# Optimization experiments

Measured on AMD Instinct MI355X. Metric: run time of the kernel, lower is better.

## Reference

```python
import jax, jax.numpy as jnp
import numpy as np
from jax import lax

B, T, D = 64, 2048, 80
H = 128          # hidden_dim
H2 = 2 * H       # conv out channels / GRU input / bi-GRU output
L = 2            # gru layers
O = 4            # output_dim


def setup_inputs() -> dict:
    key = jax.random.key(0)
    ks = jax.random.split(key, 16)
    f = lambda k, shape, scale: (jax.random.normal(k, shape) * scale).astype(jnp.float32)
    return {
        "x": f(ks[0], (B, T, D), 1.0),
        # conv branches: PyTorch Conv1d weight layout [out, in, k]
        "conv1_w": f(ks[1], (H2, D, 1), 0.1), "conv1_b": f(ks[2], (H2,), 0.1),
        "conv3_w": f(ks[3], (H2, D, 3), 0.06), "conv3_b": f(ks[4], (H2,), 0.1),
        "conv5_w": f(ks[5], (H2, D, 5), 0.05), "conv5_b": f(ks[6], (H2,), 0.1),
        # skip / head linears: PyTorch Linear weight layout [out, in]
        "fc1_w": f(ks[7], (H2, D), 0.1), "fc1_b": f(ks[8], (H2,), 0.1),
        "fc_w": f(ks[9], (O, H2), 0.06), "fc_b": f(ks[10], (O,), 0.1),
        # stacked bidirectional GRU weights: [layer, dir(0=fwd,1=bwd), 3H, ...]
        # gate order along 3H axis follows PyTorch: reset, update, new
        "gru_wih": f(ks[11], (L, 2, 3 * H, H2), 0.06),
        "gru_whh": f(ks[12], (L, 2, 3 * H, H), 0.08),
        "gru_bih": f(ks[13], (L, 2, 3 * H), 0.05),
        "gru_bhh": f(ks[14], (L, 2, 3 * H), 0.05),
    }


def _conv_relu(xc, w, b, pad):
    # xc: [B, C, T], w: [out, in, k]
    y = lax.conv_general_dilated(xc, w, window_strides=(1,), padding=[(pad, pad)],
                                 dimension_numbers=("NCH", "OIH", "NCH"))
    return jax.nn.relu(y + b[None, :, None])


def _gru_dir(xin, wih, whh, bih, bhh, reverse):
    # xin: [B, T, Din]; PyTorch GRU cell: r,z,n gate order
    Hd = whh.shape[1]
    xg = jnp.einsum("btd,gd->btg", xin, wih) + bih  # [B, T, 3H]
    if reverse:
        xg = xg[:, ::-1]

    def step(h, xt):
        hg = h @ whh.T + bhh                                   # [B, 3H]
        r = jax.nn.sigmoid(xt[:, :Hd] + hg[:, :Hd])
        z = jax.nn.sigmoid(xt[:, Hd:2 * Hd] + hg[:, Hd:2 * Hd])
        n = jnp.tanh(xt[:, 2 * Hd:] + r * hg[:, 2 * Hd:])
        hn = (1.0 - z) * n + z * h
        return hn, hn

    h0 = jnp.zeros((xin.shape[0], Hd), xin.dtype)
    _, hs = lax.scan(step, h0, xg.transpose(1, 0, 2))          # [T, B, H]
    hs = hs.transpose(1, 0, 2)
    return hs[:, ::-1] if reverse else hs


def reference(x, conv1_w, conv1_b, conv3_w, conv3_b, conv5_w, conv5_b,
              fc1_w, fc1_b, fc_w, fc_b, gru_wih, gru_whh, gru_bih, gru_bhh):
    xc = x.transpose(0, 2, 1)                                   # [B, D, T]
    oc = (_conv_relu(xc, conv1_w, conv1_b, 0)
          + _conv_relu(xc, conv3_w, conv3_b, 1)
          + _conv_relu(xc, conv5_w, conv5_b, 2))                # [B, 2H, T]
    h = oc.transpose(0, 2, 1)                                   # [B, T, 2H]

    for l in range(gru_wih.shape[0]):
        fwd = _gru_dir(h, gru_wih[l, 0], gru_whh[l, 0], gru_bih[l, 0], gru_bhh[l, 0], False)
        bwd = _gru_dir(h, gru_wih[l, 1], gru_whh[l, 1], gru_bih[l, 1], gru_bhh[l, 1], True)
        h = jnp.concatenate([fwd, bwd], axis=-1)                # [B, T, 2H]

    output_gru = h + x @ fc1_w.T + fc1_b                        # skip connection
    out = output_gru @ fc_w.T + fc_b                            # [B, T, O]
    return output_gru, out
```

## Files before the change

### kernel.cpp

```cpp
#include <hip/hip_runtime.h>
#include <hip/hip_bf16.h>
#include <hip/hip_fp16.h>

typedef _Float16 f16;
typedef _Float16 h2_t __attribute__((ext_vector_type(2)));
typedef _Float16 h4_t __attribute__((ext_vector_type(4)));
typedef _Float16 h8_t __attribute__((ext_vector_type(8)));
typedef float    f4_t __attribute__((ext_vector_type(4)));

#define B_  64
#define T_  2048
#define BT_ 131072
#define OG_ELEMS 33554432ull

__device__ __forceinline__ void gl_lds16(const void* g, void* lds) {
  __builtin_amdgcn_global_load_lds(
      (const __attribute__((address_space(1))) void*)g,
      (__attribute__((address_space(3))) void*)lds, 16, 0, 0);
}

__device__ __forceinline__ h8_t pack8(const float* p) {
  f4_t a = *(const f4_t*)p;
  f4_t b = *(const f4_t*)(p + 4);
  return h8_t{(f16)a[0], (f16)a[1], (f16)a[2], (f16)a[3],
              (f16)b[0], (f16)b[1], (f16)b[2], (f16)b[3]};
}

__device__ __forceinline__ void kloop128(
    const f16* __restrict__ Ab, int lda,
    const f16* __restrict__ Bb, int ldb,
    int ksteps, f16* As, f16* Bs, f4_t (&acc)[4][4])
{
  const int tid  = threadIdx.x;
  const int wave = tid >> 6, lane = tid & 63;
  const int srow = tid >> 2;
  const int scol = (tid & 3) * 8;
  const int fr   = lane & 15;
  const int kb   = (lane >> 4) * 8;
  const int rA   = (wave >> 1) * 64 + fr;
  const int rB   = (wave & 1) * 64 + fr;

  f16* dA0 = As + wave * 512;
  f16* dA1 = As + 2048 + wave * 512;
  f16* dB0 = Bs + wave * 512;
  f16* dB1 = Bs + 2048 + wave * 512;
  const f16* gA0 = Ab + (size_t)srow * lda + scol;
  const f16* gA1 = Ab + (size_t)(srow + 64) * lda + scol;
  const f16* gB0 = Bb + (size_t)srow * ldb + scol;
  const f16* gB1 = Bb + (size_t)(srow + 64) * ldb + scol;

  for (int kt = 0; kt < ksteps; ++kt) {
    const int ko = kt * 32;
    gl_lds16(gA0 + ko, dA0);
    gl_lds16(gA1 + ko, dA1);
    gl_lds16(gB0 + ko, dB0);
    gl_lds16(gB1 + ko, dB1);
    __syncthreads();
    h8_t af[4], bf[4];
#pragma unroll
    for (int m = 0; m < 4; m++) af[m] = *(const h8_t*)(As + (rA + m * 16) * 32 + kb);
#pragma unroll
    for (int n = 0; n < 4; n++) bf[n] = *(const h8_t*)(Bs + (rB + n * 16) * 32 + kb);
#pragma unroll
    for (int m = 0; m < 4; m++)
#pragma unroll
      for (int n = 0; n < 4; n++)
        acc[m][n] = __builtin_amdgcn_mfma_f32_16x16x32_f16(af[m], bf[n], acc[m][n], 0, 0, 0);
    __syncthreads();
  }
}

__global__ __launch_bounds__(256) void gemm_xT_kernel(
    const f16* __restrict__ A, int lda,
    const f16* __restrict__ Bw, int ldb,
    const float* __restrict__ bias,
    f16* __restrict__ out, int ksteps, int mode)
{
  __shared__ f16 As[4096];
  __shared__ f16 Bs[4096];
  f4_t acc[4][4];
#pragma unroll
  for (int m = 0; m < 4; m++)
#pragma unroll
    for (int n = 0; n < 4; n++) acc[m][n] = f4_t{0.f, 0.f, 0.f, 0.f};

  const f16* Ab = A + (size_t)blockIdx.x * 128 * lda;
  const f16* Bb = Bw + (size_t)blockIdx.y * 128 * ldb;
  kloop128(Ab, lda, Bb, ldb, ksteps, As, Bs, acc);

  const int tid = threadIdx.x, wave = tid >> 6, lane = tid & 63;
  const int col0 = blockIdx.y * 128 + (wave & 1) * 64 + (lane & 15);
  const int row0 = blockIdx.x * 128 + (wave >> 1) * 64 + (lane >> 4) * 4;
  const int b = blockIdx.x >> 4;
#pragma unroll
  for (int n = 0; n < 4; n++) {
    const int col = col0 + n * 16;
    const float bv = bias[col];
    const int g = col >> 7, jj = col & 127;
    const size_t base = (mode == 0)
        ? ((size_t)((b * 3 + g) * 128 + jj)) * 2048
        : ((size_t)((g * 64 + b) * 128 + jj)) * 2048;
#pragma unroll
    for (int m = 0; m < 4; m++) {
      const int row = row0 + m * 16;
      const int t = row & 2047;
      h4_t v = h4_t{(f16)(acc[m][n][0] + bv), (f16)(acc[m][n][1] + bv),
                    (f16)(acc[m][n][2] + bv), (f16)(acc[m][n][3] + bv)};
      *(h4_t*)(out + base + t) = v;
    }
  }
}

__global__ __launch_bounds__(256) void conv3sum_kernel(
    const f16* __restrict__ A5,
    const f16* __restrict__ W5p, const f16* __restrict__ W3p, const f16* __restrict__ W1p,
    const float* __restrict__ b5, const float* __restrict__ b3, const float* __restrict__ b1,
    f16* __restrict__ oc)
{
  __shared__ f16 As[4096];
  __shared__ f16 Bs[4096];
  const int tid = threadIdx.x, wave = tid >> 6, lane = tid & 63;
  const int col0 = blockIdx.y * 128 + (wave & 1) * 64 + (lane & 15);
  const int row0 = blockIdx.x * 128 + (wave >> 1) * 64 + (lane >> 4) * 4;
  const f16* Ab = A5 + (size_t)blockIdx.x * 128 * 480;

  f4_t tot[4][4];
#pragma unroll
  for (int m = 0; m < 4; m++)
#pragma unroll
    for (int n = 0; n < 4; n++) tot[m][n] = f4_t{0.f, 0.f, 0.f, 0.f};

  auto seg = [&](const f16* Wp, int ldb, int ks, int aoff, const float* bias) {
    f4_t acc[4][4];
#pragma unroll
    for (int m = 0; m < 4; m++)
#pragma unroll
      for (int n = 0; n < 4; n++) acc[m][n] = f4_t{0.f, 0.f, 0.f, 0.f};
    kloop128(Ab + aoff, 480, Wp + (size_t)blockIdx.y * 128 * ldb, ldb, ks, As, Bs, acc);
#pragma unroll
    for (int n = 0; n < 4; n++) {
      const float bv = bias[col0 + n * 16];
#pragma unroll
      for (int m = 0; m < 4; m++)
#pragma unroll
        for (int q = 0; q < 4; q++)
          tot[m][n][q] += fmaxf(acc[m][n][q] + bv, 0.f);
    }
  };
  seg(W5p, 480, 15, 0,   b5);
  seg(W3p, 288, 9,  96,  b3);
  seg(W1p, 96,  3,  192, b1);

#pragma unroll
  for (int n = 0; n < 4; n++) {
    const int col = col0 + n * 16;
#pragma unroll
    for (int m = 0; m < 4; m++) {
      const int row = row0 + m * 16;
#pragma unroll
      for (int q = 0; q < 4; q++)
        oc[(size_t)(row + q) * 256 + col] = (f16)tot[m][n][q];
    }
  }
}

__global__ __launch_bounds__(384) void im2col_kernel(
    const float* __restrict__ x, f16* __restrict__ A5)
{
  const int tid = threadIdx.x;
  const int r = tid / 12, c8 = tid % 12;
  const int bt = blockIdx.x * 32 + r;
  const int kg = blockIdx.y;
  const int b = bt >> 11, t = bt & 2047;
  const int ts = t + kg - 2;
  h8_t v = {0, 0, 0, 0, 0, 0, 0, 0};
  if (c8 < 10 && (unsigned)ts < 2048u) {
    const float* src = x + ((size_t)(b << 11) + ts) * 80 + c8 * 8;
    f4_t a = *(const f4_t*)src;
    f4_t bvec = *(const f4_t*)(src + 4);
    v = h8_t{(f16)a[0], (f16)a[1], (f16)a[2], (f16)a[3],
             (f16)bvec[0], (f16)bvec[1], (f16)bvec[2], (f16)bvec[3]};
  }
  *(h8_t*)(A5 + (size_t)bt * 480 + kg * 96 + c8 * 8) = v;
}

__global__ void pack_convw_kernel(
    const float* __restrict__ w1, const float* __restrict__ w3,
    const float* __restrict__ w5, const float* __restrict__ fc1w,
    f16* __restrict__ W5p, f16* __restrict__ W3p, f16* __restrict__ W1p,
    f16* __restrict__ FC1p)
{
  const int col = blockIdx.x;
  const int c = threadIdx.x;
  if (col < 480) {
    const int kg = col / 96, d = col % 96;
    W5p[c * 480 + col] = (f16)((d < 80) ? w5[(c * 80 + d) * 5 + kg] : 0.f);
  } else if (col < 768) {
    const int cc = col - 480, k = cc / 96, d = cc % 96;
    W3p[c * 288 + cc] = (f16)((d < 80) ? w3[(c * 80 + d) * 3 + k] : 0.f);
  } else if (col < 864) {
    const int d = col - 768;
    W1p[c * 96 + d] = (f16)((d < 80) ? w1[c * 80 + d] : 0.f);
  } else {
    const int d = col - 864;
    FC1p[c * 96 + d] = (f16)((d < 80) ? fc1w[c * 80 + d] : 0.f);
  }
}

__global__ void cast_f16_kernel(const float* __restrict__ src, f16* __restrict__ dst, int n8)
{
  const int i = blockIdx.x * blockDim.x + threadIdx.x;
  if (i >= n8) return;
  f4_t a = *(const f4_t*)(src + (size_t)i * 8);
  f4_t b = *(const f4_t*)(src + (size_t)i * 8 + 4);
  h8_t v = h8_t{(f16)a[0], (f16)a[1], (f16)a[2], (f16)a[3],
                (f16)b[0], (f16)b[1], (f16)b[2], (f16)b[3]};
  *(h8_t*)(dst + (size_t)i * 8) = v;
}

__device__ __forceinline__ float sigmoidf_(float x) {
  return __fdividef(1.f, 1.f + __expf(-x));
}
__device__ __forceinline__ float tanhf_(float x) {
  float e2 = __expf(-2.f * fabsf(x));
  float th = __fdividef(1.f - e2, 1.f + e2);
  return copysignf(th, x);
}

#define DOT8(acc0, acc1, hv, wv)                                                       \
  do {                                                                                 \
    acc0 = __builtin_amdgcn_fdot2(h2_t{hv[0], hv[1]}, h2_t{wv[0], wv[1]}, acc0, false);\
    acc1 = __builtin_amdgcn_fdot2(h2_t{hv[2], hv[3]}, h2_t{wv[2], wv[3]}, acc1, false);\
    acc0 = __builtin_amdgcn_fdot2(h2_t{hv[4], hv[5]}, h2_t{wv[4], wv[5]}, acc0, false);\
    acc1 = __builtin_amdgcn_fdot2(h2_t{hv[6], hv[7]}, h2_t{wv[6], wv[7]}, acc1, false);\
  } while (0)

template<int DIR, int L1>
__device__ __forceinline__ void gru_chain(
    const f16* __restrict__ xg_b,
    const f16* __restrict__ xf_b,
    const float* __restrict__ whh_d,
    const float* __restrict__ bhh_d,
    f16* __restrict__ h0_b,
    float* __restrict__ og_b)
{
  const int tid  = threadIdx.x;
  const int wv   = tid >> 6;
  const int lane = tid & 63;
  const int j    = wv * 32 + (lane >> 1);
  const int kh   = lane & 1;

  h8_t WR[8], WZ[8], WN[8];
  {
    const int co = kh * 64;
#pragma unroll
    for (int q = 0; q < 8; q++) WR[q] = pack8(whh_d + (size_t)j * 128 + co + q * 8);
#pragma unroll
    for (int q = 0; q < 8; q++) WZ[q] = pack8(whh_d + (size_t)(128 + j) * 128 + co + q * 8);
#pragma unroll
    for (int q = 0; q < 8; q++) WN[q] = pack8(whh_d + (size_t)(256 + j) * 128 + co + q * 8);
  }
  const float br = bhh_d[j], bz = bhh_d[128 + j], bn = bhh_d[256 + j];

  __shared__ __align__(16) f16 hb[2][128];
  if (tid < 128) { hb[0][tid] = (f16)0.f; hb[1][tid] = (f16)0.f; }
  float hstate = 0.f;

  h8_t xrA{}, xzA{}, xnA{}, xfA{};
  h8_t xrB{}, xzB{}, xnB{}, xfB{};
  auto ld4 = [&](int s8, h8_t& xr, h8_t& xz, h8_t& xn, h8_t& xf) {
    const int tb = DIR ? (T_ - 8 - s8) : s8;
    xr = *(const h8_t*)(xg_b + (size_t)(0 * 128 + j) * 2048 + tb);
    xz = *(const h8_t*)(xg_b + (size_t)(1 * 128 + j) * 2048 + tb);
    xn = *(const h8_t*)(xg_b + (size_t)(2 * 128 + j) * 2048 + tb);
    if (L1) xf = *(const h8_t*)(xf_b + (size_t)j * 2048 + tb);
  };
  ld4(0, xrA, xzA, xnA, xfA);
  asm volatile("s_waitcnt lgkmcnt(0)" ::: "memory");
  __builtin_amdgcn_s_barrier();
  __builtin_amdgcn_sched_barrier(0);

  for (int s8 = 0; s8 < T_; s8 += 8) {
    if ((s8 + 8) < T_) ld4(s8 + 8, xrB, xzB, xnB, xfB);
#pragma unroll
    for (int ss = 0; ss < 8; ss++) {
      const int e = DIR ? (7 - ss) : ss;
      const f16* hbuf = &hb[ss & 1][0] + kh * 64;
      h8_t hv[8];
#pragma unroll
      for (int q = 0; q < 8; q++) hv[q] = *(const h8_t*)(hbuf + q * 8);
      float r0 = 0.f, r1 = 0.f, z0 = 0.f, z1 = 0.f, n0 = 0.f, n1 = 0.f;
#pragma unroll
      for (int q = 0; q < 8; q++) {
        DOT8(r0, r1, hv[q], WR[q]);
        DOT8(z0, z1, hv[q], WZ[q]);
        DOT8(n0, n1, hv[q], WN[q]);
      }
      float sr = r0 + r1; sr += __shfl_xor(sr, 1);
      float sz = z0 + z1; sz += __shfl_xor(sz, 1);
      float sn = n0 + n1; sn += __shfl_xor(sn, 1);
      const float rr = sigmoidf_((float)xrA[e] + sr + br);
      const float zz = sigmoidf_((float)xzA[e] + sz + bz);
      const float na = (float)xnA[e] + rr * (sn + bn);
      const float th = tanhf_(na);
      hstate = (1.f - zz) * th + zz * hstate;
      const int t = DIR ? (T_ - 1 - (s8 + ss)) : (s8 + ss);
      if (!kh) {
        if (L1) og_b[(size_t)t * 256 + j] = hstate + (float)xfA[e];
        else    h0_b[(size_t)t * 256 + j] = (f16)hstate;
        hb[(ss & 1) ^ 1][j] = (f16)hstate;
      }
      asm volatile("s_waitcnt lgkmcnt(0)" ::: "memory");
      __builtin_amdgcn_s_barrier();
      __builtin_amdgcn_sched_barrier(0);
    }
    xrA = xrB; xzA = xzB; xnA = xnB;
    if (L1) xfA = xfB;
  }
}

__global__ __launch_bounds__(256, 1) void gru_rec3_kernel(
    const f16* __restrict__ xgT, const float* __restrict__ whh,
    const float* __restrict__ bhh, const f16* __restrict__ xfT,
    f16* __restrict__ h0out, float* __restrict__ ogout)
{
  const int b = blockIdx.x >> 1, d = blockIdx.x & 1;
  const f16* xg_b = xgT + (size_t)(d * 64 + b) * 3 * 128 * 2048;
  const f16* xf_b = xfT ? (xfT + (size_t)(d * 64 + b) * 128 * 2048) : nullptr;
  const float* whh_d = whh + (size_t)d * 384 * 128;
  const float* bhh_d = bhh + d * 384;
  f16* h0_b = h0out ? (h0out + (size_t)b * 2048 * 256 + d * 128) : nullptr;
  float* og_b = ogout ? (ogout + (size_t)b * 2048 * 256 + d * 128) : nullptr;

  if (ogout) {
    if (d == 0) gru_chain<0, 1>(xg_b, xf_b, whh_d, bhh_d, nullptr, og_b);
    else        gru_chain<1, 1>(xg_b, xf_b, whh_d, bhh_d, nullptr, og_b);
  } else {
    if (d == 0) gru_chain<0, 0>(xg_b, nullptr, whh_d, bhh_d, h0_b, nullptr);
    else        gru_chain<1, 0>(xg_b, nullptr, whh_d, bhh_d, h0_b, nullptr);
  }
}

__global__ __launch_bounds__(256) void fc_out_kernel(
    const float* __restrict__ og, const float* __restrict__ fcw,
    const float* __restrict__ fcb, float* __restrict__ out)
{
  const int lane = threadIdx.x & 63;
  const int wid = (blockIdx.x * 256 + threadIdx.x) >> 6;
  const int nw = (gridDim.x * 256) >> 6;
  const f4_t w0 = *(const f4_t*)(fcw + 0 * 256 + lane * 4);
  const f4_t w1 = *(const f4_t*)(fcw + 1 * 256 + lane * 4);
  const f4_t w2 = *(const f4_t*)(fcw + 2 * 256 + lane * 4);
  const f4_t w3 = *(const f4_t*)(fcw + 3 * 256 + lane * 4);
  const float b0 = fcb[0], b1 = fcb[1], b2 = fcb[2], b3 = fcb[3];
  for (int row = wid; row < BT_; row += nw) {
    const f4_t v = *(const f4_t*)(og + (size_t)row * 256 + lane * 4);
    float p0 = v[0] * w0[0] + v[1] * w0[1] + v[2] * w0[2] + v[3] * w0[3];
    float p1 = v[0] * w1[0] + v[1] * w1[1] + v[2] * w1[2] + v[3] * w1[3];
    float p2 = v[0] * w2[0] + v[1] * w2[1] + v[2] * w2[2] + v[3] * w2[3];
    float p3 = v[0] * w3[0] + v[1] * w3[1] + v[2] * w3[2] + v[3] * w3[3];
#pragma unroll
    for (int off = 1; off < 64; off <<= 1) {
      p0 += __shfl_xor(p0, off);
      p1 += __shfl_xor(p1, off);
      p2 += __shfl_xor(p2, off);
      p3 += __shfl_xor(p3, off);
    }
    if (lane == 0) {
      f4_t o4 = f4_t{p0 + b0, p1 + b1, p2 + b2, p3 + b3};
      *(f4_t*)(out + (size_t)row * 4) = o4;
    }
  }
}

extern "C" void kernel_launch(void* const* d_in, const int* in_sizes, int n_in,
                              void* d_out, int out_size, void* d_ws, size_t ws_size,
                              hipStream_t stream)
{
  const float* x       = (const float*)d_in[0];
  const float* conv1_w = (const float*)d_in[1];
  const float* conv1_b = (const float*)d_in[2];
  const float* conv3_w = (const float*)d_in[3];
  const float* conv3_b = (const float*)d_in[4];
  const float* conv5_w = (const float*)d_in[5];
  const float* conv5_b = (const float*)d_in[6];
  const float* fc1_w   = (const float*)d_in[7];
  const float* fc1_b   = (const float*)d_in[8];
  const float* fc_w    = (const float*)d_in[9];
  const float* fc_b    = (const float*)d_in[10];
  const float* gru_wih = (const float*)d_in[11];
  const float* gru_whh = (const float*)d_in[12];
  const float* gru_bih = (const float*)d_in[13];
  const float* gru_bhh = (const float*)d_in[14];

  size_t off = 0;
  auto alloc = [&](size_t bytes) {
    char* p = (char*)d_ws + off;
    off += (bytes + 255) & ~(size_t)255;
    return p;
  };
  f16* A5   = (f16*)alloc((size_t)BT_ * 480 * 2);
  f16* W5p  = (f16*)alloc(256 * 480 * 2);
  f16* W3p  = (f16*)alloc(256 * 288 * 2);
  f16* W1p  = (f16*)alloc(256 * 96 * 2);
  f16* FC1p = (f16*)alloc(256 * 96 * 2);
  f16* wihp = (f16*)alloc(4ull * 384 * 256 * 2);
  f16* oc   = (f16*)alloc((size_t)BT_ * 256 * 2);
  f16* xgT  = (f16*)alloc(2ull * 64 * 3 * 128 * 2048 * 2);
  f16* h0   = (f16*)alloc((size_t)BT_ * 256 * 2);
  f16* xfT  = (f16*)alloc(2ull * 64 * 128 * 2048 * 2);
  if (off > ws_size) return;

  float* og   = (float*)d_out;
  float* out2 = (float*)d_out + OG_ELEMS;

  im2col_kernel<<<dim3(BT_ / 32, 5), 384, 0, stream>>>(x, A5);
  pack_convw_kernel<<<960, 256, 0, stream>>>(conv1_w, conv3_w, conv5_w, fc1_w,
                                             W5p, W3p, W1p, FC1p);
  cast_f16_kernel<<<(49152 + 255) / 256, 256, 0, stream>>>(gru_wih, wihp, 49152);

  conv3sum_kernel<<<dim3(1024, 2), 256, 0, stream>>>(A5, W5p, W3p, W1p,
                                                     conv5_b, conv3_b, conv1_b, oc);
  gemm_xT_kernel<<<dim3(1024, 2), 256, 0, stream>>>(A5 + 192, 480, FC1p, 96,
                                                    fc1_b, xfT, 3, 1);

  for (int l = 0; l < 2; ++l) {
    const f16* hin = l ? h0 : oc;
    for (int d = 0; d < 2; ++d) {
      gemm_xT_kernel<<<dim3(1024, 3), 256, 0, stream>>>(
          hin, 256, wihp + (size_t)(l * 2 + d) * 384 * 256, 256,
          gru_bih + (l * 2 + d) * 384,
          xgT + (size_t)d * 64 * 3 * 128 * 2048, 8, 0);
    }
    gru_rec3_kernel<<<128, 256, 0, stream>>>(
        xgT, gru_whh + (size_t)l * 2 * 384 * 128, gru_bhh + (size_t)l * 2 * 384,
        l ? xfT : nullptr, l ? nullptr : h0, l ? og : nullptr);
  }

  fc_out_kernel<<<1024, 256, 0, stream>>>(og, fc_w, fc_b, out2);
}
```

Baseline: 2.536 ms.

## Merge both GRU directions into one 512-thread block and use DPP for lane swaps

```diff
diff --git a/kernel.cpp b/kernel.cpp
--- a/kernel.cpp
+++ b/kernel.cpp
@@ -24,6 +24,12 @@
   f4_t b = *(const f4_t*)(p + 4);
   return h8_t{(f16)a[0], (f16)a[1], (f16)a[2], (f16)a[3],
               (f16)b[0], (f16)b[1], (f16)b[2], (f16)b[3]};
+}
+
+__device__ __forceinline__ float dpp_swap1(float x) {
+  int i = __builtin_bit_cast(int, x);
+  int y = __builtin_amdgcn_update_dpp(0, i, 0xB1, 0xF, 0xF, true);
+  return __builtin_bit_cast(float, y);
 }
 
 __device__ __forceinline__ void kloop128(
@@ -235,57 +241,63 @@
     acc1 = __builtin_amdgcn_fdot2(h2_t{hv[6], hv[7]}, h2_t{wv[6], wv[7]}, acc1, false);\
   } while (0)
 
-template<int DIR, int L1>
-__device__ __forceinline__ void gru_chain(
-    const f16* __restrict__ xg_b,
-    const f16* __restrict__ xf_b,
-    const float* __restrict__ whh_d,
-    const float* __restrict__ bhh_d,
-    f16* __restrict__ h0_b,
-    float* __restrict__ og_b)
-{
+template<int L1>
+__global__ __launch_bounds__(512, 2) void gru_rec6_kernel(
+    const f16* __restrict__ xgT, const float* __restrict__ whh,
+    const float* __restrict__ bhh, const f16* __restrict__ xfT,
+    f16* __restrict__ h0out, float* __restrict__ ogout)
+{
+  const int b    = blockIdx.x;
   const int tid  = threadIdx.x;
-  const int wv   = tid >> 6;
+  const int dir  = tid >> 8;
+  const int wv   = (tid >> 6) & 3;
   const int lane = tid & 63;
   const int j    = wv * 32 + (lane >> 1);
   const int kh   = lane & 1;
 
+  const float* whh_d = whh + (size_t)dir * 49152;
+  const float* bhh_d = bhh + dir * 384;
+  const int co = kh * 64;
+
   h8_t WR[8], WZ[8], WN[8];
-  {
-    const int co = kh * 64;
-#pragma unroll
-    for (int q = 0; q < 8; q++) WR[q] = pack8(whh_d + (size_t)j * 128 + co + q * 8);
-#pragma unroll
-    for (int q = 0; q < 8; q++) WZ[q] = pack8(whh_d + (size_t)(128 + j) * 128 + co + q * 8);
-#pragma unroll
-    for (int q = 0; q < 8; q++) WN[q] = pack8(whh_d + (size_t)(256 + j) * 128 + co + q * 8);
-  }
+#pragma unroll
+  for (int q = 0; q < 8; q++) WR[q] = pack8(whh_d + (size_t)j * 128 + co + q * 8);
+#pragma unroll
+  for (int q = 0; q < 8; q++) WZ[q] = pack8(whh_d + (size_t)(128 + j) * 128 + co + q * 8);
+#pragma unroll
+  for (int q = 0; q < 8; q++) WN[q] = pack8(whh_d + (size_t)(256 + j) * 128 + co + q * 8);
   const float br = bhh_d[j], bz = bhh_d[128 + j], bn = bhh_d[256 + j];
 
-  __shared__ __align__(16) f16 hb[2][128];
-  if (tid < 128) { hb[0][tid] = (f16)0.f; hb[1][tid] = (f16)0.f; }
+  __shared__ __align__(16) f16 hb[1024];
+  hb[tid] = (f16)0.f; hb[512 + tid] = (f16)0.f;
   float hstate = 0.f;
+
+  const int me  = dir ? 7    : 0;
+  const int mt  = dir ? 2047 : 0;
+  const int mtb = dir ? 2040 : 0;
+
+  const f16* xg_b = xgT + (size_t)(dir * 64 + b) * 786432 + (size_t)j * 2048;
+  const f16* xf_b = L1 ? (xfT + (size_t)(dir * 64 + b) * 262144 + (size_t)j * 2048) : nullptr;
+  f16*   h0p = L1 ? nullptr : (h0out + (size_t)b * 524288 + dir * 128 + j);
+  float* ogp = L1 ? (ogout + (size_t)b * 524288 + dir * 128 + j) : nullptr;
 
   h8_t xrA{}, xzA{}, xnA{}, xfA{};
   h8_t xrB{}, xzB{}, xnB{}, xfB{};
   auto ld4 = [&](int s8, h8_t& xr, h8_t& xz, h8_t& xn, h8_t& xf) {
-    const int tb = DIR ? (T_ - 8 - s8) : s8;
-    xr = *(const h8_t*)(xg_b + (size_t)(0 * 128 + j) * 2048 + tb);
-    xz = *(const h8_t*)(xg_b + (size_t)(1 * 128 + j) * 2048 + tb);
-    xn = *(const h8_t*)(xg_b + (size_t)(2 * 128 + j) * 2048 + tb);
-    if (L1) xf = *(const h8_t*)(xf_b + (size_t)j * 2048 + tb);
+    const int tb = s8 ^ mtb;
+    xr = *(const h8_t*)(xg_b + tb);
+    xz = *(const h8_t*)(xg_b + 262144 + tb);
+    xn = *(const h8_t*)(xg_b + 524288 + tb);
+    if (L1) xf = *(const h8_t*)(xf_b + tb);
   };
   ld4(0, xrA, xzA, xnA, xfA);
-  asm volatile("s_waitcnt lgkmcnt(0)" ::: "memory");
-  __builtin_amdgcn_s_barrier();
-  __builtin_amdgcn_sched_barrier(0);
+  __syncthreads();
 
   for (int s8 = 0; s8 < T_; s8 += 8) {
     if ((s8 + 8) < T_) ld4(s8 + 8, xrB, xzB, xnB, xfB);
 #pragma unroll
     for (int ss = 0; ss < 8; ss++) {
-      const int e = DIR ? (7 - ss) : ss;
-      const f16* hbuf = &hb[ss & 1][0] + kh * 64;
+      const f16* hbuf = hb + dir * 512 + (ss & 1) * 128 + co;
       h8_t hv[8];
 #pragma unroll
       for (int q = 0; q < 8; q++) hv[q] = *(const h8_t*)(hbuf + q * 8);
@@ -296,19 +308,26 @@
         DOT8(z0, z1, hv[q], WZ[q]);
         DOT8(n0, n1, hv[q], WN[q]);
       }
-      float sr = r0 + r1; sr += __shfl_xor(sr, 1);
-      float sz = z0 + z1; sz += __shfl_xor(sz, 1);
-      float sn = n0 + n1; sn += __shfl_xor(sn, 1);
-      const float rr = sigmoidf_((float)xrA[e] + sr + br);
-      const float zz = sigmoidf_((float)xzA[e] + sz + bz);
-      const float na = (float)xnA[e] + rr * (sn + bn);
+      float sr = r0 + r1; sr += dpp_swap1(sr);
+      float sz = z0 + z1; sz += dpp_swap1(sz);
+      float sn = n0 + n1; sn += dpp_swap1(sn);
+      const float cxr = dir ? (float)xrA[7 - ss] : (float)xrA[ss];
+      const float cxz = dir ? (float)xzA[7 - ss] : (float)xzA[ss];
+      const float cxn = dir ? (float)xnA[7 - ss] : (float)xnA[ss];
+      const float rr = sigmoidf_(cxr + sr + br);
+      const float zz = sigmoidf_(cxz + sz + bz);
+      const float na = cxn + rr * (sn + bn);
       const float th = tanhf_(na);
       hstate = (1.f - zz) * th + zz * hstate;
-      const int t = DIR ? (T_ - 1 - (s8 + ss)) : (s8 + ss);
+      const int t = (s8 + ss) ^ mt;
       if (!kh) {
-        if (L1) og_b[(size_t)t * 256 + j] = hstate + (float)xfA[e];
-        else    h0_b[(size_t)t * 256 + j] = (f16)hstate;
-        hb[(ss & 1) ^ 1][j] = (f16)hstate;
+        if (L1) {
+          const float cxf = dir ? (float)xfA[7 - ss] : (float)xfA[ss];
+          ogp[(size_t)t * 256] = hstate + cxf;
+        } else {
+          h0p[(size_t)t * 256] = (f16)hstate;
+        }
+        hb[dir * 512 + ((ss & 1) ^ 1) * 128 + j] = (f16)hstate;
       }
       asm volatile("s_waitcnt lgkmcnt(0)" ::: "memory");
       __builtin_amdgcn_s_barrier();
@@ -316,28 +335,6 @@
     }
     xrA = xrB; xzA = xzB; xnA = xnB;
     if (L1) xfA = xfB;
-  }
-}
-
-__global__ __launch_bounds__(256, 1) void gru_rec3_kernel(
-    const f16* __restrict__ xgT, const float* __restrict__ whh,
-    const float* __restrict__ bhh, const f16* __restrict__ xfT,
-    f16* __restrict__ h0out, float* __restrict__ ogout)
-{
-  const int b = blockIdx.x >> 1, d = blockIdx.x & 1;
-  const f16* xg_b = xgT + (size_t)(d * 64 + b) * 3 * 128 * 2048;
-  const f16* xf_b = xfT ? (xfT + (size_t)(d * 64 + b) * 128 * 2048) : nullptr;
-  const float* whh_d = whh + (size_t)d * 384 * 128;
-  const float* bhh_d = bhh + d * 384;
-  f16* h0_b = h0out ? (h0out + (size_t)b * 2048 * 256 + d * 128) : nullptr;
-  float* og_b = ogout ? (ogout + (size_t)b * 2048 * 256 + d * 128) : nullptr;
-
-  if (ogout) {
-    if (d == 0) gru_chain<0, 1>(xg_b, xf_b, whh_d, bhh_d, nullptr, og_b);
-    else        gru_chain<1, 1>(xg_b, xf_b, whh_d, bhh_d, nullptr, og_b);
-  } else {
-    if (d == 0) gru_chain<0, 0>(xg_b, nullptr, whh_d, bhh_d, h0_b, nullptr);
-    else        gru_chain<1, 0>(xg_b, nullptr, whh_d, bhh_d, h0_b, nullptr);
   }
 }
 
@@ -432,9 +429,13 @@
           gru_bih + (l * 2 + d) * 384,
           xgT + (size_t)d * 64 * 3 * 128 * 2048, 8, 0);
     }
-    gru_rec3_kernel<<<128, 256, 0, stream>>>(
-        xgT, gru_whh + (size_t)l * 2 * 384 * 128, gru_bhh + (size_t)l * 2 * 384,
-        l ? xfT : nullptr, l ? nullptr : h0, l ? og : nullptr);
+    if (l == 0)
+      gru_rec6_kernel<0><<<64, 512, 0, stream>>>(
+          xgT, gru_whh, gru_bhh, nullptr, h0, nullptr);
+    else
+      gru_rec6_kernel<1><<<64, 512, 0, stream>>>(
+          xgT, gru_whh + (size_t)2 * 384 * 128, gru_bhh + 2 * 384,
+          xfT, nullptr, og);
   }
 
   fc_out_kernel<<<1024, 256, 0, stream>>>(og, fc_w, fc_b, out2);
```

Measured after the change: 3.796 ms. +49.6%, slower.
